# Optimization experiments

Hardware: AMD Instinct MI355X
Metric: run time of the kernel (lower is better)

The kernel has to match this reference:

```python
import jax, jax.numpy as jnp
import numpy as np

NEG_INF = -jnp.inf


def setup_inputs() -> dict:
    key = jax.random.key(0)
    k1, k2, k3, k4 = jax.random.split(key, 4)
    B, V = 256, 128000
    logits = jax.random.normal(k1, (B, V), dtype=jnp.float32)
    temperatures = jax.random.uniform(k2, (B,), dtype=jnp.float32, minval=0.5, maxval=1.5)
    top_ks = jax.random.randint(k3, (B,), 0, 1024, dtype=jnp.int32)
    top_ps = jax.random.uniform(k4, (B,), dtype=jnp.float32)
    return {"logits": logits, "temperatures": temperatures, "top_ks": top_ks, "top_ps": top_ps}


def _filtered_logits(logits, temperatures, top_ks, top_ps):
    # Faithful vectorized version of the per-row torch loops.
    B, V = logits.shape
    x = logits.astype(jnp.float32) / temperatures[:, None]

    # Sort each row descending once; reuse for top-k and top-p.
    order = jnp.argsort(-x, axis=-1)                       # [B, V] desc indices
    sorted_x = jnp.take_along_axis(x, order, axis=-1)      # [B, V]
    ranks = jnp.arange(V)[None, :]                         # [1, V]

    # top-k: active only when 0 < k < V (matches torch branch)
    k = top_ks[:, None].astype(jnp.int32)
    topk_active = (k > 0) & (k < V)
    keep_k = jnp.where(topk_active, ranks < k, True)
    sorted_x = jnp.where(keep_k, sorted_x, NEG_INF)

    # top-p on softmax of top-k-filtered logits. Softmax is order-preserving,
    # so sorted probs == softmax of sorted (filtered) logits.
    sorted_probs = jax.nn.softmax(sorted_x, axis=-1)
    cumsum = jnp.cumsum(sorted_probs, axis=-1)
    p = top_ps[:, None]
    cutoff = jnp.sum(cumsum <= p, axis=-1, keepdims=True)  # (cumsum<=p).sum()
    cutoff = jnp.where(cutoff < V, cutoff + 1, cutoff)     # include next token
    topp_active = (p > 0.0) & (p < 1.0)
    keep_p = jnp.where(topp_active, ranks < cutoff, True)
    sorted_x = jnp.where(keep_p, sorted_x, NEG_INF)

    # Unsort back to original token order.
    inv = jnp.argsort(order, axis=-1)
    return jnp.take_along_axis(sorted_x, inv, axis=-1)


def reference(logits, temperatures, top_ks, top_ps):
    x = _filtered_logits(logits, temperatures, top_ks, top_ps)
    probs = jax.nn.softmax(x, axis=-1)
    # Gumbel-max style sampling: argmax(probs / Exp(1)) (torch .exponential_ trick)
    e = jax.random.exponential(jax.random.key(42), probs.shape, dtype=jnp.float32)
    e = jnp.maximum(e, 1e-10)
    return jnp.argmax(probs / e, axis=-1)
```

## Files before the change

kernel.cpp:

```cpp
#include <hip/hip_runtime.h>
#include <stdint.h>

#define VV 128000
#define BLOCK 1024
#define NB 4096
#define CAP 4096
#define THR 2.0f
#define U0  0xC0000000u
#define MSEL 2048
#define NSEG 16
#define CAPSEG 320
#define F4SEG 2000

typedef unsigned long long ull;

__device__ __forceinline__ uint32_t rotl32(uint32_t x, int r){ return (x << r) | (x >> (32 - r)); }

__device__ __forceinline__ float exp_noise(uint32_t f){
  const uint32_t ks0 = 0u, ks1 = 42u, ks2 = 0x1BD11BDAu ^ 0u ^ 42u;
  uint32_t x0 = 0u + ks0;
  uint32_t x1 = f + ks1;
#define R1(r) { x0 += x1; x1 = rotl32(x1, r); x1 ^= x0; }
  R1(13) R1(15) R1(26) R1(6)   x0 += ks1; x1 += ks2 + 1u;
  R1(17) R1(29) R1(16) R1(24)  x0 += ks2; x1 += ks0 + 2u;
  R1(13) R1(15) R1(26) R1(6)   x0 += ks0; x1 += ks1 + 3u;
  R1(17) R1(29) R1(16) R1(24)  x0 += ks1; x1 += ks2 + 4u;
  R1(13) R1(15) R1(26) R1(6)   x0 += ks2; x1 += ks0 + 5u;
#undef R1
  uint32_t bits = x0 ^ x1;
  float u = __uint_as_float((bits >> 9) | 0x3F800000u) - 1.0f;
  float e = -log1pf(-u);
  return fmaxf(e, 1e-10f);
}

__device__ __forceinline__ uint32_t fkey(float x){
  uint32_t u = __float_as_uint(x);
  return u ^ ((u & 0x80000000u) ? 0xFFFFFFFFu : 0x80000000u);
}
__device__ __forceinline__ float keyval(uint32_t k){
  uint32_t bits = (k & 0x80000000u) ? (k ^ 0x80000000u) : ~k;
  return __uint_as_float(bits);
}

__device__ void suffix_scan_u(uint32_t* h, uint32_t* tmp, int tid){
  const int base = tid * 4;
  uint32_t l0=h[base], l1=h[base+1], l2=h[base+2], l3=h[base+3];
  uint32_t s3=l3, s2=l2+s3, s1=l1+s2, s0=l0+s1;
  tmp[tid] = s0; __syncthreads();
  for (int d=1; d<BLOCK; d<<=1){
    uint32_t add = (tid+d<BLOCK) ? tmp[tid+d] : 0u;
    __syncthreads();
    tmp[tid] += add;
    __syncthreads();
  }
  uint32_t E = (tid+1<BLOCK) ? tmp[tid+1] : 0u;
  h[base]=s0+E; h[base+1]=s1+E; h[base+2]=s2+E; h[base+3]=s3+E;
  __syncthreads();
}
__device__ void suffix_scan_f(float* h, float* tmp, int tid){
  const int base = tid * 4;
  float l0=h[base], l1=h[base+1], l2=h[base+2], l3=h[base+3];
  float s3=l3, s2=l2+s3, s1=l1+s2, s0=l0+s1;
  tmp[tid] = s0; __syncthreads();
  for (int d=1; d<BLOCK; d<<=1){
    float add = (tid+d<BLOCK) ? tmp[tid+d] : 0.f;
    __syncthreads();
    tmp[tid] += add;
    __syncthreads();
  }
  float E = (tid+1<BLOCK) ? tmp[tid+1] : 0.f;
  h[base]=s0+E; h[base+1]=s1+E; h[base+2]=s2+E; h[base+3]=s3+E;
  __syncthreads();
}

__device__ uint32_t select_tth_smallest(uint32_t* a, int n, int t){
  for (int i=0;i<t;i++){
    int mi=i; uint32_t mv=a[i];
    for (int j=i+1;j<n;j++) if (a[j]<mv){ mv=a[j]; mi=j; }
    a[mi]=a[i]; a[i]=mv;
  }
  return a[t-1];
}

__device__ void bitonic_sort(ull* a, int N, int tid){
  for (int len=2; len<=N; len<<=1){
    for (int j=len>>1; j>0; j>>=1){
      for (int i=tid; i<N; i+=BLOCK){
        int l = i ^ j;
        if (l > i){
          ull x = a[i], y = a[l];
          bool asc = ((i & len) == 0);
          if (asc ? (x > y) : (x < y)){ a[i]=y; a[l]=x; }
        }
      }
      __syncthreads();
    }
  }
}

#define ROW4R_BEGIN \
    for (int c0 = tid; c0 < VV/4; c0 += BLOCK*4){ \
      float4 qv[4]; int cb[4]; bool gv[4]; \
      _Pragma("unroll") \
      for (int t=0;t<4;t++){ int cc = c0 + t*BLOCK; gv[t] = (cc < VV/4); cb[t] = cc*4; if (gv[t]) qv[t] = rp[cc]; } \
      _Pragma("unroll") \
      for (int t=0;t<4;t++) if (gv[t]){ \
        float vs[4] = {qv[t].x, qv[t].y, qv[t].z, qv[t].w}; \
        _Pragma("unroll") \
        for (int j=0;j<4;j++){ \
          uint32_t u = fkey(vs[j]); \
          uint32_t idx = (uint32_t)(cb[t]+j); \
          (void)idx;
#define ROW4R_END } } }

#define ROW4_BEGIN \
    for (int c0 = tid; c0 < VV/4; c0 += BLOCK*4){ \
      float4 qv[4]; int cb[4]; bool gv[4]; \
      _Pragma("unroll") \
      for (int t=0;t<4;t++){ int cc = c0 + t*BLOCK; gv[t] = (cc < VV/4); cb[t] = cc*4; if (gv[t]) qv[t] = rp[cc]; } \
      _Pragma("unroll") \
      for (int t=0;t<4;t++) if (gv[t]){ \
        float xs[4] = {qv[t].x, qv[t].y, qv[t].z, qv[t].w}; \
        _Pragma("unroll") \
        for (int j=0;j<4;j++){ \
          float x = xs[j]/T; \
          uint32_t u = fkey(x); \
          uint32_t idx = (uint32_t)(cb[t]+j); \
          (void)idx;
#define ROW4_END } } }

__global__ __launch_bounds__(256) void gather_kernel(
    const float* __restrict__ logits, ull* __restrict__ g_cand,
    uint32_t* __restrict__ g_cnt)
{
  const int bid = blockIdx.x;
  const int row = bid >> 4, seg = bid & 15;
  const int tid = threadIdx.x;
  const float4* rp = reinterpret_cast<const float4*>(logits + (size_t)row * VV);
  __shared__ ull buf[CAPSEG];
  __shared__ int cnt;
  if (tid==0) cnt = 0;
  __syncthreads();
  const int c1 = (seg+1)*F4SEG;
  for (int c = seg*F4SEG + tid; c < c1; c += 256){
    float4 q = rp[c];
    float vs[4] = {q.x, q.y, q.z, q.w};
    #pragma unroll
    for (int j=0;j<4;j++){
      if (vs[j] >= THR){
        int pos = atomicAdd(&cnt, 1);
        uint32_t idx = (uint32_t)(c*4 + j);
        if (pos < CAPSEG) buf[pos] = (((ull)fkey(vs[j]))<<32) | (ull)(~idx);
      }
    }
  }
  __syncthreads();
  const int n = min(cnt, CAPSEG);
  ull* dst = g_cand + (size_t)row*(NSEG*CAPSEG) + seg*CAPSEG;
  for (int i=tid;i<n;i+=256) dst[i] = buf[i];
  if (tid==0) g_cnt[row*NSEG + seg] = (uint32_t)cnt;
}

__global__ __launch_bounds__(BLOCK) void sampler_kernel(
    const float* __restrict__ logits, const float* __restrict__ temps,
    const int* __restrict__ topks, const float* __restrict__ topps,
    int* __restrict__ out, const ull* __restrict__ g_cand,
    const uint32_t* __restrict__ g_cnt, int use_ws)
{
  __shared__ __align__(16) uint8_t SM[102400];
  uint32_t* hist  = (uint32_t*)SM;
  uint32_t* hsuf  = (uint32_t*)(SM + 16*1024);
  ull*      srt2  = (ull*)(SM + 32*1024);
  uint32_t* wtot  = (uint32_t*)(SM + 48*1024);
  uint32_t* h4    = (uint32_t*)SM;
  ull*      cand  = (ull*)SM;
  uint32_t* h2    = (uint32_t*)(SM + 32*1024);
  ull*      sort2 = (ull*)(SM + 48*1024);
  float*    S     = (float*)SM;
  float*    wf    = (float*)(SM + 16*1024);
  uint32_t* wu    = (uint32_t*)(SM + 64*1024);
  float*    tmpf  = (float*)(SM + 80*1024);
  uint32_t* tmpu  = (uint32_t*)(SM + 84*1024);
  float*    ck    = (float*)(SM + 88*1024);
  ull*      red   = (ull*)(SM + 92*1024);

  __shared__ int s_idx, s_n, s_n2, s_tk, s_ntk, s_tp, s_ntp;
  __shared__ uint32_t s_uk, s_idxk, s_up, s_idxp;
  __shared__ float s_m, s_Zk, s_Ztot;
  __shared__ ull s_K0;

  const int b   = blockIdx.x;
  const int tid = threadIdx.x;
  const float T = temps[b];
  const int   k = topks[b];
  const float p = topps[b];
  const float* row = logits + (size_t)b * VV;
  const float4* rp = reinterpret_cast<const float4*>(row);
  const bool topk_act = (k > 0) && (k < VV);
  const bool topp_act = (p > 0.0f) && (p < 1.0f);

  if (topk_act && use_ws && k <= BLOCK){
    int cs[NSEG]; int nf = 0; bool ovf = false;
    const uint32_t* gc = g_cnt + b*NSEG;
    #pragma unroll
    for (int s=0;s<NSEG;s++){
      int c = (int)gc[s];
      if (c > CAPSEG) ovf = true;
      c = min(c, CAPSEG);
      cs[s] = c; nf += c;
    }
    if (!ovf && nf >= k){
      const ull* gcd = g_cand + (size_t)b*(NSEG*CAPSEG);
      for (int i=tid;i<NB;i+=BLOCK) hist[i]=0u;
      __syncthreads();
      for (int s=0;s<NSEG;s++){
        for (int i=tid;i<cs[s];i+=BLOCK){
          uint32_t u2 = (uint32_t)(gcd[s*CAPSEG+i]>>32);
          uint32_t bu = (u2 - U0) >> 12; if (bu > 4095u) bu = 4095u;
          atomicAdd(&hist[bu], 1u);
        }
      }
      __syncthreads();
      const int lane = tid & 63, wid = tid >> 6;
      const int bb = tid*4;
      uint32_t l0=hist[bb], l1=hist[bb+1], l2=hist[bb+2], l3=hist[bb+3];
      uint32_t s3=l3, s2=l2+s3, s1=l1+s2, s0=l0+s1;
      uint32_t v = s0;
      #pragma unroll
      for (int d=1; d<64; d<<=1){ uint32_t o=__shfl_down(v,d); if (lane+d<64) v += o; }
      if (lane==0) wtot[wid] = v;
      const uint32_t wexcl = v - s0;
      __syncthreads();
      if (wid==0){
        uint32_t w = (lane<16) ? wtot[lane] : 0u;
        uint32_t own = w;
        #pragma unroll
        for (int d=1; d<16; d<<=1){ uint32_t o=__shfl_down(w,d); if (lane+d<16) w += o; }
        if (lane<16) wtot[lane] = w - own;
      }
      __syncthreads();
      const uint32_t E = wtot[wid] + wexcl;
      hsuf[bb]=s0+E; hsuf[bb+1]=s1+E; hsuf[bb+2]=s2+E; hsuf[bb+3]=s3+E;
      if (tid==0) s_idx = 0;
      __syncthreads();
      #pragma unroll
      for (int j=0;j<4;j++){
        int i = bb+j;
        uint32_t a  = hsuf[i];
        uint32_t nn = (i < NB-1) ? hsuf[i+1] : 0u;
        if (a >= (uint32_t)k && nn < (uint32_t)k) s_idx = i;
      }
      __syncthreads();
      const int gam = s_idx;
      const int m = (int)hsuf[gam];
      if (m <= MSEL){
        for (int s=0;s<NSEG;s++){
          for (int i=tid;i<cs[s];i+=BLOCK){
            ull e = gcd[s*CAPSEG+i];
            uint32_t u2 = (uint32_t)(e>>32);
            uint32_t bu = (u2 - U0) >> 12; if (bu > 4095u) bu = 4095u;
            if ((int)bu >= gam){
              uint32_t sub  = atomicSub(&hist[bu], 1u) - 1u;
              uint32_t base = (bu < NB-1) ? hsuf[bu+1] : 0u;
              srt2[base + sub] = e;
            }
          }
        }
        __syncthreads();
        ull K0=0ull, K1=0ull; int r0=0, r1=0;
        if (tid < m){
          K0 = srt2[tid];
          uint32_t u2 = (uint32_t)(K0>>32);
          uint32_t bu = (u2 - U0) >> 12; if (bu > 4095u) bu = 4095u;
          uint32_t base = (bu < NB-1) ? hsuf[bu+1] : 0u;
          uint32_t nb = hsuf[bu] - base;
          int r = (int)base;
          for (uint32_t q=0;q<nb;q++) r += (srt2[base+q] > K0);
          r0 = r;
        }
        if (tid+BLOCK < m){
          K1 = srt2[tid+BLOCK];
          uint32_t u2 = (uint32_t)(K1>>32);
          uint32_t bu = (u2 - U0) >> 12; if (bu > 4095u) bu = 4095u;
          uint32_t base = (bu < NB-1) ? hsuf[bu+1] : 0u;
          uint32_t nb = hsuf[bu] - base;
          int r = (int)base;
          for (uint32_t q=0;q<nb;q++) r += (srt2[base+q] > K1);
          r1 = r;
        }
        if (tid < m && r0 == 0)       s_K0 = K0;
        if (tid+BLOCK < m && r1 == 0) s_K0 = K1;
        __syncthreads();
        const float xm = keyval((uint32_t)(s_K0>>32)) / T;
        float w0 = 0.f, w1 = 0.f;
        if (tid < m && r0 < k)       w0 = expf(keyval((uint32_t)(K0>>32))/T - xm);
        if (tid+BLOCK < m && r1 < k) w1 = expf(keyval((uint32_t)(K1>>32))/T - xm);
        ck[tid] = 0.f;
        __syncthreads();
        if (tid < m && r0 < k)       ck[r0] = w0;
        if (tid+BLOCK < m && r1 < k) ck[r1] = w1;
        __syncthreads();
        for (int d=BLOCK/2; d>0; d>>=1){
          if (tid < d) ck[tid] += ck[tid+d];
          __syncthreads();
        }
        if (tid==0) s_Ztot = ck[0];
        __syncthreads();
        const float Zk = s_Ztot;
        ck[tid] = 0.f;
        __syncthreads();
        if (tid < m && r0 < k)       ck[r0] = w0 / Zk;
        if (tid+BLOCK < m && r1 < k) ck[r1] = w1 / Zk;
        __syncthreads();
        for (int d=1; d<BLOCK; d<<=1){
          float add = (tid >= d) ? ck[tid-d] : 0.f;
          __syncthreads();
          ck[tid] += add;
          __syncthreads();
        }
        tmpu[tid] = (tid < k && ck[tid] <= p) ? 1u : 0u;
        __syncthreads();
        for (int d=BLOCK/2; d>0; d>>=1){
          if (tid < d) tmpu[tid] += tmpu[tid+d];
          __syncthreads();
        }
        int L;
        if (!topp_act) L = k;
        else { int c = (int)tmpu[0]; L = (c >= k) ? k : (c + 1); }
        red[tid] = 0ull;
        __syncthreads();
        if (tid < m && r0 < L){
          uint32_t idx0 = ~(uint32_t)K0;
          float q = w0 / exp_noise((uint32_t)b * (uint32_t)VV + idx0);
          red[r0] = (((ull)__float_as_uint(q)) << 32) | (uint32_t)K0;
        }
        if (tid+BLOCK < m && r1 < L){
          uint32_t idx1 = ~(uint32_t)K1;
          float q = w1 / exp_noise((uint32_t)b * (uint32_t)VV + idx1);
          red[r1] = (((ull)__float_as_uint(q)) << 32) | (uint32_t)K1;
        }
        __syncthreads();
        for (int d=BLOCK/2; d>0; d>>=1){
          if (tid < d){ ull o = red[tid+d]; if (o > red[tid]) red[tid] = o; }
          __syncthreads();
        }
        if (tid==0) out[b] = (int)(~(uint32_t)(red[0] & 0xFFFFFFFFull));
        return;
      }
      __syncthreads();
    }
  }

  if (topk_act){
    for (int i=tid;i<4*NB;i+=BLOCK) h4[i]=0u;
    __syncthreads();
    ROW4R_BEGIN
      atomicAdd(&h4[((u>>20)<<2) | (uint32_t)(tid&3)], 1u);
    ROW4R_END
    __syncthreads();
    for (int i=tid;i<NB;i+=BLOCK)
      wu[i] = h4[(i<<2)] + h4[(i<<2)|1] + h4[(i<<2)|2] + h4[(i<<2)|3];
    __syncthreads();
    suffix_scan_u(wu, tmpu, tid);
    if (tid==0) s_idx = 0;
    __syncthreads();
    for (int i=tid;i<NB;i+=BLOCK){
      uint32_t a  = wu[i];
      uint32_t nn = (i+1<NB) ? wu[i+1] : 0u;
      if (a >= (uint32_t)k && nn < (uint32_t)k) s_idx = i;
    }
    __syncthreads();
    const uint32_t beta = (uint32_t)s_idx;
    const int n = (int)wu[beta];
    const uint32_t c_above = (beta+1<NB) ? wu[beta+1] : 0u;
    if (n <= CAP){
      if (tid==0) s_n = 0;
      __syncthreads();
      ROW4R_BEGIN
        if ((u>>20) >= beta){
          int pos = atomicAdd(&s_n, 1);
          cand[pos] = (((ull)(~u))<<32) | idx;
        }
      ROW4R_END
      __syncthreads();
      ull* srt; int m;
      if (n <= 1024){ srt = cand; m = n; }
      else {
        for (int i=tid;i<NB;i+=BLOCK) h2[i]=0u;
        __syncthreads();
        for (int i=tid;i<n;i+=BLOCK){
          uint32_t u2 = ~(uint32_t)(cand[i]>>32);
          if ((u2>>20) == beta) atomicAdd(&h2[(u2>>8)&0xFFFu], 1u);
        }
        __syncthreads();
        suffix_scan_u(h2, tmpu, tid);
        const uint32_t kr = (uint32_t)k - c_above;
        if (tid==0) s_idx = 0;
        __syncthreads();
        for (int i=tid;i<NB;i+=BLOCK){
          uint32_t a  = h2[i];
          uint32_t nn = (i+1<NB) ? h2[i+1] : 0u;
          if (a >= kr && nn < kr) s_idx = i;
        }
        __syncthreads();
        const uint32_t gam = (uint32_t)s_idx;
        const int np = (int)(c_above + h2[gam]);
        if (np <= 1024){
          if (tid==0) s_n2 = 0;
          __syncthreads();
          const uint32_t cut24 = (beta<<12) | gam;
          for (int i=tid;i<n;i+=BLOCK){
            ull e = cand[i];
            uint32_t u2 = ~(uint32_t)(e>>32);
            if ((u2>>8) >= cut24){
              int pos = atomicAdd(&s_n2, 1);
              sort2[pos] = e;
            }
          }
          __syncthreads();
          srt = sort2; m = np;
        } else { srt = cand; m = n; }
      }
      int N = 2; while (N < m) N <<= 1;
      for (int i=tid;i<N;i+=BLOCK) if (i >= m) srt[i] = 0xFFFFFFFFFFFFFFFFull;
      __syncthreads();
      bitonic_sort(srt, N, tid);
      const int kk = k;
      const float xm = keyval(~(uint32_t)(srt[0]>>32)) / T;
      float w = 0.f; uint32_t myidx = 0u;
      if (tid < kk){
        ull e = srt[tid];
        myidx = (uint32_t)e;
        float xv = keyval(~(uint32_t)(e>>32)) / T;
        w = expf(xv - xm);
      }
      ck[tid] = w; __syncthreads();
      for (int d=BLOCK/2; d>0; d>>=1){
        if (tid < d) ck[tid] += ck[tid+d];
        __syncthreads();
      }
      if (tid==0) s_Ztot = ck[0];
      __syncthreads();
      const float Zk = s_Ztot;
      ck[tid] = w / Zk; __syncthreads();
      for (int d=1; d<BLOCK; d<<=1){
        float add = (tid >= d) ? ck[tid-d] : 0.f;
        __syncthreads();
        ck[tid] += add;
        __syncthreads();
      }
      tmpu[tid] = (tid < kk && ck[tid] <= p) ? 1u : 0u;
      __syncthreads();
      for (int d=BLOCK/2; d>0; d>>=1){
        if (tid < d) tmpu[tid] += tmpu[tid+d];
        __syncthreads();
      }
      int L;
      if (!topp_act) L = kk;
      else { int c = (int)tmpu[0]; L = (c >= kk) ? kk : (c + 1); }
      ull best = 0ull;
      if (tid < L){
        float q = w / exp_noise((uint32_t)b * (uint32_t)VV + myidx);
        best = (((ull)__float_as_uint(q)) << 32) | (uint32_t)(~myidx);
      }
      red[tid] = best; __syncthreads();
      for (int d=BLOCK/2; d>0; d>>=1){
        if (tid < d){ ull o = red[tid+d]; if (o > red[tid]) red[tid] = o; }
        __syncthreads();
      }
      if (tid==0) out[b] = (int)(~(uint32_t)(red[0] & 0xFFFFFFFFull));
      return;
    }
    __syncthreads();
  }

  for (int i=tid;i<NB;i+=BLOCK){ S[i]=0.f; wu[i]=0u; }
  __syncthreads();
  float lmax = -3.4e38f;
  ROW4_BEGIN
    lmax = fmaxf(lmax, x);
    atomicAdd(&wu[u>>20], 1u);
    atomicAdd(&S[u>>20], expf(x));
  ROW4_END
  tmpf[tid] = lmax; __syncthreads();
  for (int d=BLOCK/2; d>0; d>>=1){
    if (tid < d) tmpf[tid] = fmaxf(tmpf[tid], tmpf[tid+d]);
    __syncthreads();
  }
  if (tid==0) s_m = tmpf[0];
  __syncthreads();
  suffix_scan_u(wu, tmpu, tid);
  suffix_scan_f(S,  tmpf, tid);

  uint32_t uk = 0u, idxk = 0xFFFFFFFFu;
  int bk1 = -1;
  if (topk_act){
    if (tid==0) s_idx = 0;
    __syncthreads();
    for (int i=tid;i<NB;i+=BLOCK){
      uint32_t a  = wu[i];
      uint32_t nn = (i+1<NB) ? wu[i+1] : 0u;
      if (a >= (uint32_t)k && nn < (uint32_t)k) s_idx = i;
    }
    __syncthreads();
    bk1 = s_idx;
    const uint32_t c_above1 = (bk1+1<NB) ? wu[bk1+1] : 0u;
    const float    M_above1 = (bk1+1<NB) ? S[bk1+1]  : 0.f;
    __syncthreads();
    for (int i=tid;i<NB;i+=BLOCK){ wu[i]=0u; wf[i]=0.f; }
    __syncthreads();
    ROW4_BEGIN
      if ((int)(u>>20) == bk1){
        atomicAdd(&wu[(u>>8)&0xFFFu], 1u);
        atomicAdd(&wf[(u>>8)&0xFFFu], expf(x));
      }
    ROW4_END
    __syncthreads();
    suffix_scan_u(wu, tmpu, tid);
    suffix_scan_f(wf, tmpf, tid);
    if (tid==0) s_idx = 0;
    __syncthreads();
    for (int i=tid;i<NB;i+=BLOCK){
      uint32_t a  = c_above1 + wu[i];
      uint32_t nn = c_above1 + ((i+1<NB) ? wu[i+1] : 0u);
      if (a >= (uint32_t)k && nn < (uint32_t)k) s_idx = i;
    }
    __syncthreads();
    const int bk2 = s_idx;
    const uint32_t c_above2 = c_above1 + ((bk2+1<NB) ? wu[bk2+1] : 0u);
    const float    M_above2 = M_above1 + ((bk2+1<NB) ? wf[bk2+1] : 0.f);
    __syncthreads();
    if (tid < 256){ wu[tid]=0u; wf[tid]=0.f; }
    __syncthreads();
    const uint32_t top24k = (((uint32_t)bk1)<<12) | (uint32_t)bk2;
    ROW4_BEGIN
      if ((u>>8) == top24k){
        atomicAdd(&wu[u & 0xFFu], 1u);
        atomicAdd(&wf[u & 0xFFu], expf(x));
      }
    ROW4_END
    __syncthreads();
    if (tid==0){
      uint32_t r = 0u; float mr = 0.f; int b3 = 0;
      for (int i=255;i>=0;--i){
        if (c_above2 + r + wu[i] >= (uint32_t)k){ b3 = i; break; }
        r += wu[i]; mr += wf[i];
      }
      const uint32_t cgt = c_above2 + r;
      const float mgt = M_above2 + mr;
      const int nt = (int)wu[b3];
      const int tk = k - (int)cgt;
      s_uk  = (((uint32_t)bk1)<<20) | (((uint32_t)bk2)<<8) | (uint32_t)b3;
      s_tk  = tk; s_ntk = nt;
      s_Zk  = mgt + (float)tk * expf(keyval(s_uk));
      s_n   = 0;
    }
    __syncthreads();
    uk = s_uk;
    if (s_tk < s_ntk){
      ROW4_BEGIN
        if (u == uk){
          int pos = atomicAdd(&s_n, 1);
          if (pos < NB) wu[pos] = idx;
        }
      ROW4_END
      __syncthreads();
      if (tid==0){
        int n2 = min(s_n, NB);
        int t  = min(s_tk, n2);
        s_idxk = select_tth_smallest(wu, n2, t);
      }
      __syncthreads();
      idxk = s_idxk;
    }
  }
  const float Zk = topk_act ? s_Zk : S[0];

  uint32_t up = 0u, idxp = 0xFFFFFFFFu;
  const float tgt = p * Zk;
  const bool pall = (!topp_act) || (tgt >= Zk);
  if (!pall){
    if (tid==0) s_idx = -2;
    __syncthreads();
    for (int i=tid;i<NB;i+=BLOCK){
      if (i > bk1){
        float a  = S[i];
        float nn = (i+1<NB) ? S[i+1] : 0.f;
        if (a > tgt && nn <= tgt) s_idx = i;
      }
    }
    __syncthreads();
    int bp1 = (s_idx >= 0) ? s_idx : bk1;
    if (bp1 < 0) bp1 = 0;
    const float Mab = (bp1+1<NB) ? S[bp1+1] : 0.f;
    __syncthreads();
    for (int i=tid;i<NB;i+=BLOCK) wf[i]=0.f;
    __syncthreads();
    ROW4_BEGIN
      if ((int)(u>>20) == bp1){
        bool kk_ok = (!topk_act) || (u > uk) || (u == uk && idx <= idxk);
        if (kk_ok) atomicAdd(&wf[(u>>8)&0xFFFu], expf(x));
      }
    ROW4_END
    __syncthreads();
    suffix_scan_f(wf, tmpf, tid);
    if (tid==0) s_idx = -2;
    __syncthreads();
    for (int i=tid;i<NB;i+=BLOCK){
      float a  = Mab + wf[i];
      float nn = Mab + ((i+1<NB) ? wf[i+1] : 0.f);
      if (a > tgt && nn <= tgt) s_idx = i;
    }
    __syncthreads();
    int bp2;
    if (s_idx >= 0){ bp2 = s_idx; }
    else {
      if (tid==0) s_idx = NB;
      __syncthreads();
      for (int i=tid;i<NB;i+=BLOCK){
        float a  = wf[i];
        float nn = (i+1<NB) ? wf[i+1] : 0.f;
        if (a > nn) atomicMin(&s_idx, i);
      }
      __syncthreads();
      bp2 = (s_idx < NB) ? s_idx : 0;
    }
    const float Mab2 = Mab + ((bp2+1<NB) ? wf[bp2+1] : 0.f);
    __syncthreads();
    if (tid < 256){ wf[tid]=0.f; wu[tid]=0u; }
    __syncthreads();
    const uint32_t top24p = (((uint32_t)bp1)<<12) | (uint32_t)bp2;
    ROW4_BEGIN
      if ((u>>8) == top24p){
        bool kk_ok = (!topk_act) || (u > uk) || (u == uk && idx <= idxk);
        if (kk_ok){
          atomicAdd(&wf[u & 0xFFu], expf(x));
          atomicAdd(&wu[u & 0xFFu], 1u);
        }
      }
    ROW4_END
    __syncthreads();
    if (tid==0){
      float run = 0.f; int b3 = -1; float mgt = 0.f;
      for (int i=255;i>=0;--i){
        float sufn = run; run += wf[i];
        if (Mab2 + run > tgt && Mab2 + sufn <= tgt){ b3 = i; mgt = Mab2 + sufn; break; }
      }
      if (b3 < 0){
        float run2 = 0.f;
        for (int i=255;i>=0;--i){
          if (wu[i] > 0u){ b3 = i; mgt = Mab2 + run2; }
          run2 += wf[i];
        }
        if (b3 < 0){ b3 = 0; mgt = Mab2; }
      }
      const uint32_t upv = (((uint32_t)bp1)<<20) | (((uint32_t)bp2)<<8) | (uint32_t)b3;
      const int ntp = (int)wu[b3];
      const float ev = expf(keyval(upv));
      int t = 0;
      for (int j=1;j<=ntp;j++){
        float before = mgt + (float)(j-1) * ev;
        if (before / Zk <= p) t++; else break;
      }
      if (t < 1) t = 1;
      s_up = upv; s_tp = t; s_ntp = ntp; s_n = 0;
    }
    __syncthreads();
    up = s_up;
    if (s_tp < s_ntp){
      ROW4_BEGIN
        if (u == up){
          bool kk_ok = (!topk_act) || (u > uk) || (u == uk && idx <= idxk);
          if (kk_ok){
            int pos = atomicAdd(&s_n, 1);
            if (pos < NB) wu[pos] = idx;
          }
        }
      ROW4_END
      __syncthreads();
      if (tid==0){
        int n2 = min(s_n, NB);
        int t  = min(s_tp, n2);
        s_idxp = select_tth_smallest(wu, n2, t);
      }
      __syncthreads();
      idxp = s_idxp;
    }
  }

  const float m  = s_m;
  const float Zs = Zk * expf(-m);
  ull best = 0ull;
  ROW4_BEGIN
    bool kk_ok = (!topk_act) || (u > uk) || (u == uk && idx <= idxk);
    bool kp_ok = pall || (u > up) || (u == up && idx <= idxp);
    if (kk_ok && kp_ok){
      float q = (expf(x - m) / Zs) / exp_noise((uint32_t)b * (uint32_t)VV + idx);
      ull pk = (((ull)__float_as_uint(q)) << 32) | (uint32_t)(~idx);
      best = (pk > best) ? pk : best;
    }
  ROW4_END
  red[tid] = best; __syncthreads();
  for (int d=BLOCK/2; d>0; d>>=1){
    if (tid < d){ ull o = red[tid+d]; if (o > red[tid]) red[tid] = o; }
    __syncthreads();
  }
  if (tid==0) out[b] = (int)(~(uint32_t)(red[0] & 0xFFFFFFFFull));
}

extern "C" void kernel_launch(void* const* d_in, const int* in_sizes, int n_in,
                              void* d_out, int out_size, void* d_ws, size_t ws_size,
                              hipStream_t stream) {
  (void)in_sizes; (void)n_in; (void)out_size;
  const float* logits = (const float*)d_in[0];
  const float* temps  = (const float*)d_in[1];
  const int*   ks     = (const int*)d_in[2];
  const float* ps     = (const float*)d_in[3];
  int* out = (int*)d_out;

  const size_t cnt_bytes  = 256 * NSEG * sizeof(uint32_t);
  const size_t cand_bytes = (size_t)256 * NSEG * CAPSEG * sizeof(ull);
  const size_t need = cnt_bytes + cand_bytes;

  uint32_t* g_cnt  = (uint32_t*)d_ws;
  ull*      g_cand = (ull*)((uint8_t*)d_ws + cnt_bytes);
  const int use_ws = (d_ws != nullptr && ws_size >= need) ? 1 : 0;

  if (use_ws)
    gather_kernel<<<256*NSEG, 256, 0, stream>>>(logits, g_cand, g_cnt);
  sampler_kernel<<<256, BLOCK, 0, stream>>>(logits, temps, ks, ps, out,
                                            g_cand, g_cnt, use_ws);
}
```

Measured before the change: 212.0 us.

## Replace block-wide shared-memory reductions with single-wavefront shuffle scans in fast path

The top-k fast path previously ran several block-wide tree reductions and a Hillis-Steele scan over shared memory, each step followed by a __syncthreads across 1024 threads. Now candidates are scattered by rank into a padded shared array, and one 64-lane wavefront processes 16 ranks per lane. It computes the normaliser, the cumulative probabilities, the top-p cutoff and the Gumbel argmax with register math and wave shuffles. Segment counts are also staged once in shared memory, and the candidate loops are flattened into a single strided loop. This removes many barriers, but the final stage runs serially on one wave and float summation order changes, which could shift cutoff decisions at borderline cases.

```diff
diff --git a/kernel.cpp b/kernel.cpp
--- a/kernel.cpp
+++ b/kernel.cpp
@@ -172,6 +172,7 @@
   uint32_t* hsuf  = (uint32_t*)(SM + 16*1024);
   ull*      srt2  = (ull*)(SM + 32*1024);
   uint32_t* wtot  = (uint32_t*)(SM + 48*1024);
+  ull*      ordx  = (ull*)(SM + 50*1024);
   uint32_t* h4    = (uint32_t*)SM;
   ull*      cand  = (ull*)SM;
   uint32_t* h2    = (uint32_t*)(SM + 32*1024);
@@ -188,6 +189,7 @@
   __shared__ uint32_t s_uk, s_idxk, s_up, s_idxp;
   __shared__ float s_m, s_Zk, s_Ztot;
   __shared__ ull s_K0;
+  __shared__ uint32_t s_cs[NSEG];
 
   const int b   = blockIdx.x;
   const int tid = threadIdx.x;
@@ -200,22 +202,25 @@
   const bool topp_act = (p > 0.0f) && (p < 1.0f);
 
   if (topk_act && use_ws && k <= BLOCK){
-    int cs[NSEG]; int nf = 0; bool ovf = false;
-    const uint32_t* gc = g_cnt + b*NSEG;
+    if (tid < NSEG) s_cs[tid] = g_cnt[b*NSEG + tid];
+    __syncthreads();
+    int cs[1]; (void)cs;
+    int nf = 0; bool ovf = false;
     #pragma unroll
     for (int s=0;s<NSEG;s++){
-      int c = (int)gc[s];
+      int c = (int)s_cs[s];
       if (c > CAPSEG) ovf = true;
-      c = min(c, CAPSEG);
-      cs[s] = c; nf += c;
+      nf += min(c, CAPSEG);
     }
     if (!ovf && nf >= k){
       const ull* gcd = g_cand + (size_t)b*(NSEG*CAPSEG);
       for (int i=tid;i<NB;i+=BLOCK) hist[i]=0u;
       __syncthreads();
-      for (int s=0;s<NSEG;s++){
-        for (int i=tid;i<cs[s];i+=BLOCK){
-          uint32_t u2 = (uint32_t)(gcd[s*CAPSEG+i]>>32);
+      for (int i=tid;i<NSEG*CAPSEG;i+=BLOCK){
+        int s = i / CAPSEG;
+        int j = i - s*CAPSEG;
+        if (j < (int)min(s_cs[s],(uint32_t)CAPSEG)){
+          uint32_t u2 = (uint32_t)(gcd[i]>>32);
           uint32_t bu = (u2 - U0) >> 12; if (bu > 4095u) bu = 4095u;
           atomicAdd(&hist[bu], 1u);
         }
@@ -254,9 +259,11 @@
       const int gam = s_idx;
       const int m = (int)hsuf[gam];
       if (m <= MSEL){
-        for (int s=0;s<NSEG;s++){
-          for (int i=tid;i<cs[s];i+=BLOCK){
-            ull e = gcd[s*CAPSEG+i];
+        for (int i=tid;i<NSEG*CAPSEG;i+=BLOCK){
+          int s = i / CAPSEG;
+          int j = i - s*CAPSEG;
+          if (j < (int)min(s_cs[s],(uint32_t)CAPSEG)){
+            ull e = gcd[i];
             uint32_t u2 = (uint32_t)(e>>32);
             uint32_t bu = (u2 - U0) >> 12; if (bu > 4095u) bu = 4095u;
             if ((int)bu >= gam){
@@ -267,84 +274,80 @@
           }
         }
         __syncthreads();
-        ull K0=0ull, K1=0ull; int r0=0, r1=0;
         if (tid < m){
-          K0 = srt2[tid];
+          ull K0 = srt2[tid];
           uint32_t u2 = (uint32_t)(K0>>32);
           uint32_t bu = (u2 - U0) >> 12; if (bu > 4095u) bu = 4095u;
           uint32_t base = (bu < NB-1) ? hsuf[bu+1] : 0u;
           uint32_t nb = hsuf[bu] - base;
           int r = (int)base;
           for (uint32_t q=0;q<nb;q++) r += (srt2[base+q] > K0);
-          r0 = r;
+          if (r < k){ ordx[r + (r>>4)] = K0; if (r == 0) s_K0 = K0; }
         }
         if (tid+BLOCK < m){
-          K1 = srt2[tid+BLOCK];
+          ull K1 = srt2[tid+BLOCK];
           uint32_t u2 = (uint32_t)(K1>>32);
           uint32_t bu = (u2 - U0) >> 12; if (bu > 4095u) bu = 4095u;
           uint32_t base = (bu < NB-1) ? hsuf[bu+1] : 0u;
           uint32_t nb = hsuf[bu] - base;
           int r = (int)base;
           for (uint32_t q=0;q<nb;q++) r += (srt2[base+q] > K1);
-          r1 = r;
-        }
-        if (tid < m && r0 == 0)       s_K0 = K0;
-        if (tid+BLOCK < m && r1 == 0) s_K0 = K1;
-        __syncthreads();
-        const float xm = keyval((uint32_t)(s_K0>>32)) / T;
-        float w0 = 0.f, w1 = 0.f;
-        if (tid < m && r0 < k)       w0 = expf(keyval((uint32_t)(K0>>32))/T - xm);
-        if (tid+BLOCK < m && r1 < k) w1 = expf(keyval((uint32_t)(K1>>32))/T - xm);
-        ck[tid] = 0.f;
-        __syncthreads();
-        if (tid < m && r0 < k)       ck[r0] = w0;
-        if (tid+BLOCK < m && r1 < k) ck[r1] = w1;
-        __syncthreads();
-        for (int d=BLOCK/2; d>0; d>>=1){
-          if (tid < d) ck[tid] += ck[tid+d];
-          __syncthreads();
-        }
-        if (tid==0) s_Ztot = ck[0];
-        __syncthreads();
-        const float Zk = s_Ztot;
-        ck[tid] = 0.f;
-        __syncthreads();
-        if (tid < m && r0 < k)       ck[r0] = w0 / Zk;
-        if (tid+BLOCK < m && r1 < k) ck[r1] = w1 / Zk;
-        __syncthreads();
-        for (int d=1; d<BLOCK; d<<=1){
-          float add = (tid >= d) ? ck[tid-d] : 0.f;
-          __syncthreads();
-          ck[tid] += add;
-          __syncthreads();
-        }
-        tmpu[tid] = (tid < k && ck[tid] <= p) ? 1u : 0u;
-        __syncthreads();
-        for (int d=BLOCK/2; d>0; d>>=1){
-          if (tid < d) tmpu[tid] += tmpu[tid+d];
-          __syncthreads();
-        }
-        int L;
-        if (!topp_act) L = k;
-        else { int c = (int)tmpu[0]; L = (c >= k) ? k : (c + 1); }
-        red[tid] = 0ull;
-        __syncthreads();
-        if (tid < m && r0 < L){
-          uint32_t idx0 = ~(uint32_t)K0;
-          float q = w0 / exp_noise((uint32_t)b * (uint32_t)VV + idx0);
-          red[r0] = (((ull)__float_as_uint(q)) << 32) | (uint32_t)K0;
-        }
-        if (tid+BLOCK < m && r1 < L){
-          uint32_t idx1 = ~(uint32_t)K1;
-          float q = w1 / exp_noise((uint32_t)b * (uint32_t)VV + idx1);
-          red[r1] = (((ull)__float_as_uint(q)) << 32) | (uint32_t)K1;
-        }
-        __syncthreads();
-        for (int d=BLOCK/2; d>0; d>>=1){
-          if (tid < d){ ull o = red[tid+d]; if (o > red[tid]) red[tid] = o; }
-          __syncthreads();
-        }
-        if (tid==0) out[b] = (int)(~(uint32_t)(red[0] & 0xFFFFFFFFull));
+          if (r < k){ ordx[r + (r>>4)] = K1; if (r == 0) s_K0 = K1; }
+        }
+        __syncthreads();
+        if (tid < 64){
+          const int kk = k;
+          const float xm = keyval((uint32_t)(s_K0>>32)) / T;
+          const int base = tid*16;
+          float wv[16]; uint32_t lo[16];
+          float tot = 0.f;
+          #pragma unroll
+          for (int q=0;q<16;q++){
+            int r = base+q;
+            float w = 0.f; uint32_t l = 0u;
+            if (r < kk){
+              ull K = ordx[r + (r>>4)];
+              w = expf(keyval((uint32_t)(K>>32))/T - xm);
+              l = (uint32_t)K;
+            }
+            wv[q]=w; lo[q]=l; tot += w;
+          }
+          float run = tot;
+          #pragma unroll
+          for (int d=1; d<64; d<<=1){ float o=__shfl_up(run,d); if (tid>=d) run += o; }
+          const float Zk = __shfl(run, 63);
+          float ctot = 0.f; float cks[16];
+          #pragma unroll
+          for (int q=0;q<16;q++){ ctot += wv[q]/Zk; cks[q] = ctot; }
+          float crun = ctot;
+          #pragma unroll
+          for (int d=1; d<64; d<<=1){ float o=__shfl_up(crun,d); if (tid>=d) crun += o; }
+          const float cexl = crun - ctot;
+          int cnt = 0;
+          #pragma unroll
+          for (int q=0;q<16;q++){
+            int r = base+q;
+            if (r < kk && (cks[q]+cexl) <= p) cnt++;
+          }
+          #pragma unroll
+          for (int d=1; d<64; d<<=1) cnt += __shfl_xor(cnt, d);
+          int L;
+          if (!topp_act) L = kk;
+          else L = (cnt >= kk) ? kk : (cnt + 1);
+          ull best = 0ull;
+          #pragma unroll
+          for (int q=0;q<16;q++){
+            int r = base+q;
+            if (r < L){
+              float qv = wv[q] / exp_noise((uint32_t)b * (uint32_t)VV + (~lo[q]));
+              ull pk = (((ull)__float_as_uint(qv)) << 32) | (ull)lo[q];
+              if (pk > best) best = pk;
+            }
+          }
+          #pragma unroll
+          for (int d=1; d<64; d<<=1){ ull o = __shfl_xor(best, d); if (o > best) best = o; }
+          if (tid==0) out[b] = (int)(~(uint32_t)(best & 0xFFFFFFFFull));
+        }
         return;
       }
       __syncthreads();
```

After: 211.8 us. About the same (-0.1%).
